# Kernel tuning notes

Measured on AMD Instinct MI355X. Metric: run time of the kernel, lower is better.

The kernel has to match this reference:

```python
import jax, jax.numpy as jnp
import numpy as np

CODEBOOK_SIZE = 8192
TOKEN_SIZE = 256
COMMITMENT_COST = 0.25


def setup_inputs() -> dict:
    key = jax.random.key(0)
    k1, k2 = jax.random.split(key)
    z = jax.random.normal(k1, (32, 1024, TOKEN_SIZE), dtype=jnp.float32)
    # embedding initialized uniform in [-1/K, 1/K] as in torch module
    embedding = jax.random.uniform(
        k2, (CODEBOOK_SIZE, TOKEN_SIZE), dtype=jnp.float32,
        minval=-1.0 / CODEBOOK_SIZE, maxval=1.0 / CODEBOOK_SIZE)
    return {"z": z, "embedding": embedding}


def reference(z, embedding):
    B, T, D = z.shape
    zf = z.reshape(B * T, D)                               # [N, D]
    # squared euclidean distances: ||z||^2 + ||e||^2 - 2 z.e
    d = (jnp.sum(zf * zf, axis=1, keepdims=True)
         + jnp.sum(embedding * embedding, axis=1)
         - 2.0 * jnp.einsum('nd,kd->nk', zf, embedding))   # [N, K]
    idx = jnp.argmin(d, axis=1)                            # [N]
    z_q = embedding[idx].reshape(B, T, D)                  # codebook gather
    commitment_loss = COMMITMENT_COST * jnp.mean(
        (jax.lax.stop_gradient(z_q) - z) ** 2)
    codebook_loss = jnp.mean((z_q - jax.lax.stop_gradient(z)) ** 2)
    loss = commitment_loss + codebook_loss                 # ema_update=False
    # straight-through estimator
    z_q_st = z + jax.lax.stop_gradient(z_q - z)
    return (z_q_st, loss, commitment_loss, codebook_loss,
            idx.reshape(B, T))
```

## Files before the change

kernel.cpp:

```cpp
#include <hip/hip_runtime.h>
#include <hip/hip_bf16.h>
#include <cfloat>

#define N_TOK   32768
#define K_CODES 8192
#define D_DIM   256
#define BTOK    128
#define CHUNK   128
#define NSPLIT  4
#define SPLITK  (K_CODES / NSPLIT)
#define CTAU_M  3.0e-5f
#define CAND_MM 2.4e-5f
#define MAXCAND 16
#define RBTOK   32
#define NRS     8
#define RSPLIT  (K_CODES / NRS)

typedef __attribute__((ext_vector_type(4)))  short bf16x4;
typedef __attribute__((ext_vector_type(8)))  short bf16x8;
typedef __attribute__((ext_vector_type(16))) float f32x16;


__device__ __forceinline__ float np_sumsq256(const float* __restrict__ row) {
    #pragma clang fp contract(off)
    float blk[2];
    #pragma unroll
    for (int b = 0; b < 2; b++) {
        const float* x = row + b * 128;
        float r[8];
        #pragma unroll
        for (int j = 0; j < 8; j++) { float v = x[j]; r[j] = v * v; }
        for (int i = 8; i < 128; i += 8) {
            #pragma unroll
            for (int j = 0; j < 8; j++) { float v = x[i + j]; r[j] += v * v; }
        }
        blk[b] = ((r[0] + r[1]) + (r[2] + r[3])) + ((r[4] + r[5]) + (r[6] + r[7]));
    }
    return blk[0] + blk[1];
}

__device__ __forceinline__ float np_einsum256(const float* __restrict__ a,
                                              const float* __restrict__ b) {
    #pragma clang fp contract(off)
    float A0 = 0.f, A1 = 0.f, A2 = 0.f, A3 = 0.f;
    for (int m = 0; m < 256; m += 16) {
        A0 = a[m+ 0]*b[m+ 0] + (a[m+ 4]*b[m+ 4] + (a[m+ 8]*b[m+ 8] + (a[m+12]*b[m+12] + A0)));
        A1 = a[m+ 1]*b[m+ 1] + (a[m+ 5]*b[m+ 5] + (a[m+ 9]*b[m+ 9] + (a[m+13]*b[m+13] + A1)));
        A2 = a[m+ 2]*b[m+ 2] + (a[m+ 6]*b[m+ 6] + (a[m+10]*b[m+10] + (a[m+14]*b[m+14] + A2)));
        A3 = a[m+ 3]*b[m+ 3] + (a[m+ 7]*b[m+ 7] + (a[m+11]*b[m+11] + (a[m+15]*b[m+15] + A3)));
    }
    return (A0 + A1) + (A2 + A3);
}

__device__ __forceinline__ float np_dtilde(float Cn, float e2k, float g) {
    #pragma clang fp contract(off)
    float t = Cn + e2k;
    float d = t - 2.0f * g;
    return d;
}

__device__ __forceinline__ unsigned short bf16_rne(float f) {
    unsigned u = __float_as_uint(f);
    unsigned r = u + 0x7fffu + ((u >> 16) & 1u);
    return (unsigned short)(r >> 16);
}
__device__ __forceinline__ void split_bf16(float f, short& hi, short& lo) {
    unsigned short h = bf16_rne(f);
    hi = (short)h;
    float hf = __uint_as_float(((unsigned)h) << 16);
    lo = (short)bf16_rne(f - hf);
}
__device__ __forceinline__ bf16x8 lo8(bf16x8 h, float4 a, float4 b) {
    float f[8] = {a.x, a.y, a.z, a.w, b.x, b.y, b.z, b.w};
    bf16x8 r;
    #pragma unroll
    for (int i = 0; i < 8; i += 2) {
        float d0 = f[i]     - __uint_as_float(((unsigned)(unsigned short)h[i])     << 16);
        float d1 = f[i + 1] - __uint_as_float(((unsigned)(unsigned short)h[i + 1]) << 16);
        __hip_bfloat162 p = __float22bfloat162_rn(make_float2(d0, d1));
        unsigned u; __builtin_memcpy(&u, &p, 4);
        r[i]     = (short)(u & 0xffffu);
        r[i + 1] = (short)(u >> 16);
    }
    return r;
}

#define MFMA3(A, ah, al, bh, bl) \
    A = __builtin_amdgcn_mfma_f32_32x32x16_bf16(ah, bh, A, 0, 0, 0); \
    A = __builtin_amdgcn_mfma_f32_32x32x16_bf16(ah, bl, A, 0, 0, 0); \
    A = __builtin_amdgcn_mfma_f32_32x32x16_bf16(al, bh, A, 0, 0, 0);

__global__ __launch_bounds__(256) void prep_e_kernel(
    const float* __restrict__ emb, float* __restrict__ e2np,
    float* __restrict__ e2h, unsigned* __restrict__ ccount,
    double* __restrict__ loss_sum)
{
    int k = blockIdx.x * 256 + threadIdx.x;
    float v = np_sumsq256(emb + (size_t)k * D_DIM);
    e2np[k] = v;
    e2h[k]  = 0.5f * v;
    if (k == 0) { *ccount = 0u; *loss_sum = 0.0; }
}

__global__ __launch_bounds__(256) void prep_z_kernel(
    const float* __restrict__ z, float* __restrict__ Cnp)
{
    int t = blockIdx.x * 256 + threadIdx.x;
    Cnp[t] = np_sumsq256(z + (size_t)t * D_DIM);
}

__global__ __launch_bounds__(256) void cvt_e_kernel(
    const float* __restrict__ src, short* __restrict__ hi, short* __restrict__ lo)
{
    size_t p = ((size_t)blockIdx.x * 256 + threadIdx.x) * 8;
    float4 v0 = *(const float4*)(src + p);
    float4 v1 = *(const float4*)(src + p + 4);
    short h[8], l[8];
    split_bf16(v0.x, h[0], l[0]); split_bf16(v0.y, h[1], l[1]);
    split_bf16(v0.z, h[2], l[2]); split_bf16(v0.w, h[3], l[3]);
    split_bf16(v1.x, h[4], l[4]); split_bf16(v1.y, h[5], l[5]);
    split_bf16(v1.z, h[6], l[6]); split_bf16(v1.w, h[7], l[7]);
    bf16x8 vh = {h[0],h[1],h[2],h[3],h[4],h[5],h[6],h[7]};
    bf16x8 vl = {l[0],l[1],l[2],l[3],l[4],l[5],l[6],l[7]};
    *(bf16x8*)(hi + p) = vh;
    *(bf16x8*)(lo + p) = vl;
}

__global__ __launch_bounds__(256) void cvt_zhi_kernel(
    const float* __restrict__ src, short* __restrict__ hi)
{
    size_t p = ((size_t)blockIdx.x * 256 + threadIdx.x) * 8;
    float4 v0 = *(const float4*)(src + p);
    float4 v1 = *(const float4*)(src + p + 4);
    bf16x8 vh = {(short)bf16_rne(v0.x), (short)bf16_rne(v0.y),
                 (short)bf16_rne(v0.z), (short)bf16_rne(v0.w),
                 (short)bf16_rne(v1.x), (short)bf16_rne(v1.y),
                 (short)bf16_rne(v1.z), (short)bf16_rne(v1.w)};
    *(bf16x8*)(hi + p) = vh;
}

#define B_ESH 0
#define B_ESL 4096
#define B_ZSH 8192
#define B_ZSL 12288
#define TILE1 1024

__global__ __launch_bounds__(512, 4) void bulk_kernel(
    const float* __restrict__ zf, const short* __restrict__ zhi,
    const short* __restrict__ ehi, const short* __restrict__ elo,
    const float* __restrict__ e2h,
    float* __restrict__ m1a, float* __restrict__ m2a, int* __restrict__ i1a)
{
    __shared__ __align__(16) short smem[2][16384];
    __shared__ float e2sall[SPLITK];
    __shared__ float s1m[BTOK], s2m[BTOK];
    __shared__ int   i1m[BTOK];

    const int tid  = threadIdx.x;
    const int lane = tid & 63;
    const int w    = tid >> 6;
    const int wt   = w & 1;
    const int wc   = w >> 1;
    const int g     = blockIdx.x & 255;
    const int split = blockIdx.x >> 8;
    const int tok0  = g * BTOK;
    const int cs0   = split * SPLITK;

    const int r0 = tid >> 2, q0 = tid & 3;
    const int so0 = r0 * 32 + ((q0 ^ ((r0 >> 1) & 3)) << 3);

    const int l31 = lane & 31, hh = lane >> 5;
    const int swz = (l31 >> 1) & 3;
    const int arow = (wc * 32 + l31) * 32;
    const int brow = (wt * 64 + l31) * 32;
    const int a0 = arow + ((hh ^ swz) << 3);
    const int a1 = arow + (((2 + hh) ^ swz) << 3);
    const int b0 = brow + ((hh ^ swz) << 3);
    const int b1 = brow + (((2 + hh) ^ swz) << 3);

    float m1[2] = {-FLT_MAX, -FLT_MAX}, m2[2] = {-FLT_MAX, -FLT_MAX};
    int   k1[2] = {0x7fffffff, 0x7fffffff};

    bf16x8 ehA, elA, zhA;  float4 zfaA, zfbA;
    bf16x8 ehB, elB, zhB;  float4 zfaB, zfbB;

    f32x16 acc[2];
    #pragma unroll
    for (int j = 0; j < 2; j++)
        #pragma unroll
        for (int r = 0; r < 16; r++) acc[j][r] = 0.f;

    const int NST = (SPLITK / CHUNK) * 8;

    auto ISSUE_A = [&](int s) {
        const int code0 = cs0 + (s >> 3) * CHUNK;
        const int d0 = (s & 7) * 32;
        const size_t ei = ((size_t)(code0 + r0) << 8) + d0 + (q0 << 3);
        const size_t zi = ((size_t)(tok0 + r0) << 8) + d0 + (q0 << 3);
        ehA = *(const bf16x8*)(ehi + ei);
        elA = *(const bf16x8*)(elo + ei);
        zhA = *(const bf16x8*)(zhi + zi);
        zfaA = *(const float4*)(zf + zi);
        zfbA = *(const float4*)(zf + zi + 4);
    };
    auto ISSUE_B = [&](int s) {
        const int code0 = cs0 + (s >> 3) * CHUNK;
        const int d0 = (s & 7) * 32;
        const size_t ei = ((size_t)(code0 + r0) << 8) + d0 + (q0 << 3);
        const size_t zi = ((size_t)(tok0 + r0) << 8) + d0 + (q0 << 3);
        ehB = *(const bf16x8*)(ehi + ei);
        elB = *(const bf16x8*)(elo + ei);
        zhB = *(const bf16x8*)(zhi + zi);
        zfaB = *(const float4*)(zf + zi);
        zfbB = *(const float4*)(zf + zi + 4);
    };

    auto STORE_A = [&](int buf) {
        bf16x8 zl0 = lo8(zhA, zfaA, zfbA);
        short* sm = smem[buf];
        *(bf16x8*)(sm + B_ESH + so0) = ehA;
        *(bf16x8*)(sm + B_ESL + so0) = elA;
        *(bf16x8*)(sm + B_ZSH + so0) = zhA;
        *(bf16x8*)(sm + B_ZSL + so0) = zl0;
    };
    auto STORE_B = [&](int buf) {
        bf16x8 zl0 = lo8(zhB, zfaB, zfbB);
        short* sm = smem[buf];
        *(bf16x8*)(sm + B_ESH + so0) = ehB;
        *(bf16x8*)(sm + B_ESL + so0) = elB;
        *(bf16x8*)(sm + B_ZSH + so0) = zhB;
        *(bf16x8*)(sm + B_ZSL + so0) = zl0;
    };

    #pragma unroll
    for (int i = 0; i < SPLITK / 512; i++) {
        int idx = tid + i * 512;
        e2sall[idx] = e2h[cs0 + idx];
    }
    ISSUE_A(0);
    ISSUE_B(1);
    STORE_A(0);
    __syncthreads();

    #pragma unroll 2
    for (int s = 0; s < NST; s++) {
        const int cur = s & 1;
        if (s + 2 < NST) {
            if (cur == 0) ISSUE_A(s + 2); else ISSUE_B(s + 2);
        }
        {
            const short* sm = smem[cur];
            {
                bf16x8 ah  = *(const bf16x8*)(sm + B_ESH + a0);
                bf16x8 al  = *(const bf16x8*)(sm + B_ESL + a0);
                bf16x8 b0h = *(const bf16x8*)(sm + B_ZSH + b0);
                bf16x8 b0l = *(const bf16x8*)(sm + B_ZSL + b0);
                bf16x8 b1h = *(const bf16x8*)(sm + B_ZSH + TILE1 + b0);
                bf16x8 b1l = *(const bf16x8*)(sm + B_ZSL + TILE1 + b0);
                MFMA3(acc[0], ah, al, b0h, b0l);
                MFMA3(acc[1], ah, al, b1h, b1l);
            }
            {
                bf16x8 ah  = *(const bf16x8*)(sm + B_ESH + a1);
                bf16x8 al  = *(const bf16x8*)(sm + B_ESL + a1);
                bf16x8 b0h = *(const bf16x8*)(sm + B_ZSH + b1);
                bf16x8 b0l = *(const bf16x8*)(sm + B_ZSL + b1);
                bf16x8 b1h = *(const bf16x8*)(sm + B_ZSH + TILE1 + b1);
                bf16x8 b1l = *(const bf16x8*)(sm + B_ZSL + TILE1 + b1);
                MFMA3(acc[0], ah, al, b0h, b0l);
                MFMA3(acc[1], ah, al, b1h, b1l);
            }
        }
        if ((s & 7) == 7) {
            const int code0 = cs0 + (s >> 3) * CHUNK;
            const float* e2c = e2sall + (s >> 3) * CHUNK;
            float ev[16];
            #pragma unroll
            for (int r = 0; r < 16; r++)
                ev[r] = e2c[wc * 32 + hh * 4 + (r & 3) + ((r >> 2) << 3)];
            #pragma unroll
            for (int tt = 0; tt < 2; tt++) {
                #pragma unroll
                for (int r = 0; r < 16; r++) {
                    float a = acc[tt][r] - ev[r];
                    int code = code0 + wc * 32 + hh * 4 + (r & 3) + ((r >> 2) << 3);
                    if (a > m1[tt]) { m2[tt] = m1[tt]; m1[tt] = a; k1[tt] = code; }
                    else if (a > m2[tt]) m2[tt] = a;
                }
            }
            #pragma unroll
            for (int j = 0; j < 2; j++)
                #pragma unroll
                for (int r = 0; r < 16; r++) acc[j][r] = 0.f;
        }
        if (s + 1 < NST) {
            if (cur == 0) STORE_B(cur ^ 1); else STORE_A(cur ^ 1);
        }
        asm volatile("s_waitcnt lgkmcnt(0)" ::: "memory");
        __builtin_amdgcn_s_barrier();
        __builtin_amdgcn_sched_barrier(0);
    }

    #pragma unroll
    for (int tt = 0; tt < 2; tt++) {
        float o1 = __shfl_xor(m1[tt], 32);
        float o2 = __shfl_xor(m2[tt], 32);
        int   oi = __shfl_xor(k1[tt], 32);
        bool take = (o1 > m1[tt]) || (o1 == m1[tt] && oi < k1[tt]);
        float w1 = take ? o1 : m1[tt];
        int   wi = take ? oi : k1[tt];
        float ls = take ? m1[tt] : o1;
        m2[tt] = fmaxf(fmaxf(m2[tt], o2), ls);
        m1[tt] = w1; k1[tt] = wi;
    }
    __syncthreads();
    if (wc == 0 && lane < 32) {
        #pragma unroll
        for (int tt = 0; tt < 2; tt++) {
            int tl = wt * 64 + tt * 32 + lane;
            s1m[tl] = m1[tt]; s2m[tl] = m2[tt]; i1m[tl] = k1[tt];
        }
    }
    __syncthreads();
    #pragma unroll
    for (int mw = 1; mw < 3; mw++) {
        if (wc == mw && lane < 32) {
            #pragma unroll
            for (int tt = 0; tt < 2; tt++) {
                int tl = wt * 64 + tt * 32 + lane;
                float a1 = s1m[tl], a2 = s2m[tl]; int ai = i1m[tl];
                bool take = (a1 > m1[tt]) || (a1 == m1[tt] && ai < k1[tt]);
                float w1 = take ? a1 : m1[tt];
                int   wi = take ? ai : k1[tt];
                float ls = take ? m1[tt] : a1;
                float w2 = fmaxf(fmaxf(m2[tt], a2), ls);
                s1m[tl] = w1; s2m[tl] = w2; i1m[tl] = wi;
            }
        }
        __syncthreads();
    }
    if (wc == 3 && lane < 32) {
        #pragma unroll
        for (int tt = 0; tt < 2; tt++) {
            int tl = wt * 64 + tt * 32 + lane;
            float a1 = s1m[tl], a2 = s2m[tl]; int ai = i1m[tl];
            bool take = (a1 > m1[tt]) || (a1 == m1[tt] && ai < k1[tt]);
            float w1 = take ? a1 : m1[tt];
            int   wi = take ? ai : k1[tt];
            float ls = take ? m1[tt] : a1;
            float w2 = fmaxf(fmaxf(m2[tt], a2), ls);
            size_t t = (size_t)(tok0 + tl) * NSPLIT + split;
            m1a[t] = w1; m2a[t] = w2; i1a[t] = wi;
        }
    }
}

__global__ __launch_bounds__(256) void merge_kernel(
    const float* __restrict__ m1a, const float* __restrict__ m2a,
    const int* __restrict__ i1a, float* __restrict__ m1f,
    int* __restrict__ idxf, int* __restrict__ clist,
    unsigned* __restrict__ ccount, unsigned* __restrict__ ccnt_g)
{
    int t = blockIdx.x * 256 + threadIdx.x;
    ccnt_g[t] = 0u;
    float w1 = m1a[t * NSPLIT], w2 = m2a[t * NSPLIT];
    int   wi = i1a[t * NSPLIT];
    #pragma unroll
    for (int s = 1; s < NSPLIT; s++) {
        float a1 = m1a[t * NSPLIT + s], a2 = m2a[t * NSPLIT + s];
        int   ai = i1a[t * NSPLIT + s];
        bool take = (a1 > w1) || (a1 == w1 && ai < wi);
        float n1 = take ? a1 : w1;
        int   ni = take ? ai : wi;
        float ls = take ? w1 : a1;
        w2 = fmaxf(fmaxf(w2, a2), ls);
        w1 = n1; wi = ni;
    }
    idxf[t] = wi; m1f[t] = w1;
    if (w1 - w2 < CTAU_M) {
        unsigned p = atomicAdd(ccount, 1u);
        clist[p] = t;
    }
}

#define R_ESH 0
#define R_ESL 4096
#define R_ZSH 8192
#define R_ZSL 9216

__global__ __launch_bounds__(256) void rescue_kernel(
    const float* __restrict__ zf, const short* __restrict__ zhi,
    const short* __restrict__ ehi, const short* __restrict__ elo,
    const float* __restrict__ e2h, const float* __restrict__ m1f,
    const unsigned* __restrict__ ccount, const int* __restrict__ clist,
    unsigned* __restrict__ ccnt_g, int* __restrict__ cand_g)
{
    const unsigned count = *ccount;
    const unsigned base  = blockIdx.x * RBTOK;
    if (base >= count) return;
    const int nt = min(RBTOK, (int)(count - base));
    const int sp = blockIdx.y;

    __shared__ __align__(16) short rsm[10240];
    __shared__ int   tls[RBTOK];
    __shared__ float thr[RBTOK];
    __shared__ float e2s[CHUNK];

    const int tid  = threadIdx.x;
    const int lane = tid & 63;
    const int w    = tid >> 6;

    if (tid < RBTOK) {
        int s = (tid < nt) ? tid : (nt - 1);
        int t = clist[base + s];
        tls[tid] = t;
        thr[tid] = (tid < nt) ? (m1f[t] - CAND_MM) : FLT_MAX;
    }
    __syncthreads();

    const int l31 = lane & 31, hh = lane >> 5;
    const float mythr = thr[l31];
    const int   mytok = tls[l31];
    const int swz = (l31 >> 1) & 3;
    const int arow = (w * 32 + l31) * 32;
    const int brow = l31 * 32;
    const int a0 = arow + ((hh ^ swz) << 3);
    const int a1 = arow + (((2 + hh) ^ swz) << 3);
    const int b0 = brow + ((hh ^ swz) << 3);
    const int b1 = brow + (((2 + hh) ^ swz) << 3);

    const int er0 = tid >> 2, eq0 = tid & 3;
    const int er1 = er0 + 64;
    const int eso0 = er0 * 32 + ((eq0 ^ ((er0 >> 1) & 3)) << 3);
    const int eso1 = er1 * 32 + ((eq0 ^ ((er1 >> 1) & 3)) << 3);
    const int zr = (tid & 127) >> 2, zq = tid & 3;
    const int zso = zr * 32 + ((zq ^ ((zr >> 1) & 3)) << 3);

    for (int c = 0; c < RSPLIT / CHUNK; c++) {
        const int code0 = sp * RSPLIT + c * CHUNK;
        const float e2v = (tid < CHUNK) ? e2h[code0 + tid] : 0.f;
        f32x16 acc;
        #pragma unroll
        for (int r = 0; r < 16; r++) acc[r] = 0.f;

        for (int st = 0; st < 8; st++) {
            const int d0 = st * 32;
            const size_t ei0 = ((size_t)(code0 + er0) << 8) + d0 + (eq0 << 3);
            const size_t ei1 = ((size_t)(code0 + er1) << 8) + d0 + (eq0 << 3);
            bf16x8 eh0 = *(const bf16x8*)(ehi + ei0);
            bf16x8 el0 = *(const bf16x8*)(elo + ei0);
            bf16x8 eh1 = *(const bf16x8*)(ehi + ei1);
            bf16x8 el1 = *(const bf16x8*)(elo + ei1);
            bf16x8 zh = {}, zl = {};
            if (tid < 128) {
                const size_t zi = ((size_t)tls[zr] << 8) + d0 + (zq << 3);
                zh = *(const bf16x8*)(zhi + zi);
                float4 za = *(const float4*)(zf + zi);
                float4 zb = *(const float4*)(zf + zi + 4);
                zl = lo8(zh, za, zb);
            }
            __syncthreads();
            *(bf16x8*)(rsm + R_ESH + eso0) = eh0;
            *(bf16x8*)(rsm + R_ESL + eso0) = el0;
            *(bf16x8*)(rsm + R_ESH + eso1) = eh1;
            *(bf16x8*)(rsm + R_ESL + eso1) = el1;
            if (tid < 128) {
                *(bf16x8*)(rsm + R_ZSH + zso) = zh;
                *(bf16x8*)(rsm + R_ZSL + zso) = zl;
            }
            if (st == 0 && tid < CHUNK) e2s[tid] = e2v;
            __syncthreads();
            {
                bf16x8 ah = *(const bf16x8*)(rsm + R_ESH + a0);
                bf16x8 al = *(const bf16x8*)(rsm + R_ESL + a0);
                bf16x8 bh = *(const bf16x8*)(rsm + R_ZSH + b0);
                bf16x8 bl = *(const bf16x8*)(rsm + R_ZSL + b0);
                MFMA3(acc, ah, al, bh, bl);
            }
            {
                bf16x8 ah = *(const bf16x8*)(rsm + R_ESH + a1);
                bf16x8 al = *(const bf16x8*)(rsm + R_ESL + a1);
                bf16x8 bh = *(const bf16x8*)(rsm + R_ZSH + b1);
                bf16x8 bl = *(const bf16x8*)(rsm + R_ZSL + b1);
                MFMA3(acc, ah, al, bh, bl);
            }
        }
        #pragma unroll
        for (int r = 0; r < 16; r++) {
            const int local = w * 32 + hh * 4 + (r & 3) + ((r >> 2) << 3);
            float a = acc[r] - e2s[local];
            if (a >= mythr) {
                unsigned p = atomicAdd(&ccnt_g[mytok], 1u);
                if (p < MAXCAND) cand_g[(size_t)mytok * MAXCAND + p] = code0 + local;
            }
        }
    }
}

__global__ __launch_bounds__(256) void resolve_kernel(
    const float* __restrict__ z, const float* __restrict__ emb,
    const float* __restrict__ e2np, const float* __restrict__ Cnp,
    const unsigned* __restrict__ ccount, const int* __restrict__ clist,
    const unsigned* __restrict__ ccnt_g, const int* __restrict__ cand_g,
    int* __restrict__ idxf)
{
    const unsigned count = *ccount;
    const int lane = threadIdx.x & 63;
    const int w    = threadIdx.x >> 6;
    for (unsigned c = blockIdx.x * 4 + w; c < count; c += gridDim.x * 4) {
        const int t = clist[c];
        const int n = (int)min(ccnt_g[t], (unsigned)MAXCAND);
        float bd = FLT_MAX; int bk = 0x7fffffff;
        if (lane < n) {
            const int k = cand_g[(size_t)t * MAXCAND + lane];
            float g = np_einsum256(z + (size_t)t * D_DIM, emb + (size_t)k * D_DIM);
            bd = np_dtilde(Cnp[t], e2np[k], g);
            bk = k;
        }
        #pragma unroll
        for (int off = 32; off >= 1; off >>= 1) {
            float od = __shfl_xor(bd, off);
            int   ok = __shfl_xor(bk, off);
            if (od < bd || (od == bd && ok < bk)) { bd = od; bk = ok; }
        }
        if (lane == 0 && n > 0) idxf[t] = bk;
    }
}

__global__ __launch_bounds__(256) void out_loss_kernel(
    const float* __restrict__ z, const float* __restrict__ emb,
    const int* __restrict__ idxf, float* __restrict__ out0,
    double* __restrict__ loss_sum)
{
    const int total4 = N_TOK * (D_DIM / 4);
    double lsum = 0.0;
    for (int p = blockIdx.x * 256 + threadIdx.x; p < total4; p += gridDim.x * 256) {
        const int n  = p >> 6;
        const int d4 = p & 63;
        const int k  = idxf[n];
        float4 zv = ((const float4*)z)[p];
        float4 ev = ((const float4*)(emb + (size_t)k * D_DIM))[d4];
        float dx = ev.x - zv.x, dy = ev.y - zv.y,
              dz = ev.z - zv.z, dw = ev.w - zv.w;
        float4 o;
        o.x = zv.x + dx; o.y = zv.y + dy; o.z = zv.z + dz; o.w = zv.w + dw;
        ((float4*)out0)[p] = o;
        lsum += (double)dx * dx + (double)dy * dy
              + (double)dz * dz + (double)dw * dw;
    }
    #pragma unroll
    for (int off = 32; off >= 1; off >>= 1) lsum += __shfl_xor(lsum, off);
    __shared__ double wsum[4];
    const int wv = threadIdx.x >> 6;
    if ((threadIdx.x & 63) == 0) wsum[wv] = lsum;
    __syncthreads();
    if (threadIdx.x == 0)
        atomicAdd(loss_sum, wsum[0] + wsum[1] + wsum[2] + wsum[3]);
}

__global__ __launch_bounds__(256) void finalize_kernel(
    const int* __restrict__ idxf, const double* __restrict__ loss_sum,
    float* __restrict__ out)
{
    const int t = blockIdx.x * 256 + threadIdx.x;
    if (t < N_TOK) out[8388611 + t] = (float)idxf[t];
    if (t == 0) {
        double mse = *loss_sum * (1.0 / 8388608.0);
        out[8388608] = (float)(1.25 * mse);
        out[8388609] = (float)(0.25 * mse);
        out[8388610] = (float)mse;
    }
}

extern "C" void kernel_launch(void* const* d_in, const int* in_sizes, int n_in,
                              void* d_out, int out_size, void* d_ws, size_t ws_size,
                              hipStream_t stream)
{
    const float* z   = (const float*)d_in[0];
    const float* emb = (const float*)d_in[1];
    float* out = (float*)d_out;
    char*  ws  = (char*)d_ws;
    char*  ob  = (char*)d_out;

    short*    ehi    = (short*)(ob + 0);
    short*    elo    = (short*)(ob + 4194304);
    short*    zhi    = (short*)(ob + 8388608);
    float*    m1a    = (float*)(ob + 25165824);
    float*    m2a    = (float*)(ob + 25690112);
    int*      i1a    = (int*)(ob + 26214400);
    int*      cand_g = (int*)(ob + 26738688);

    double*   loss_sum = (double*)(ws + 0);
    unsigned* ccount   = (unsigned*)(ws + 8);
    float*    e2np     = (float*)(ws + 16);
    float*    e2h      = (float*)(ws + 32784);
    float*    Cnp      = (float*)(ws + 65552);
    float*    m1f      = (float*)(ws + 196624);
    int*      idxf     = (int*)(ws + 327696);
    int*      clist    = (int*)(ws + 458768);
    unsigned* ccnt_g   = (unsigned*)(ws + 589840);

    prep_e_kernel<<<dim3(K_CODES / 256), dim3(256), 0, stream>>>(
        emb, e2np, e2h, ccount, loss_sum);
    prep_z_kernel<<<dim3(N_TOK / 256), dim3(256), 0, stream>>>(z, Cnp);
    cvt_e_kernel<<<dim3(K_CODES * D_DIM / 8 / 256), dim3(256), 0, stream>>>(emb, ehi, elo);
    cvt_zhi_kernel<<<dim3(N_TOK * D_DIM / 8 / 256), dim3(256), 0, stream>>>(z, zhi);
    bulk_kernel<<<dim3((N_TOK / BTOK) * NSPLIT), dim3(512), 0, stream>>>(
        z, zhi, ehi, elo, e2h, m1a, m2a, i1a);
    merge_kernel<<<dim3(N_TOK / 256), dim3(256), 0, stream>>>(
        m1a, m2a, i1a, m1f, idxf, clist, ccount, ccnt_g);
    rescue_kernel<<<dim3(N_TOK / RBTOK, NRS), dim3(256), 0, stream>>>(
        z, zhi, ehi, elo, e2h, m1f, ccount, clist, ccnt_g, cand_g);
    resolve_kernel<<<dim3(128), dim3(256), 0, stream>>>(
        z, emb, e2np, Cnp, ccount, clist, ccnt_g, cand_g, idxf);
    out_loss_kernel<<<dim3(1024), dim3(256), 0, stream>>>(
        z, emb, idxf, out, loss_sum);
    finalize_kernel<<<dim3(N_TOK / 256), dim3(256), 0, stream>>>(
        idxf, loss_sum, out);
}
```

Baseline: 780.0 us.

## Restructure bulk distance kernel to 256 threads, 2x2 MFMA tiles, three codebook splits

Reworks the main distance/argmin kernel from 512-thread blocks with 4 codebook splits to 256-thread blocks with 3 uneven splits (22/21/21 chunks), giving 768 blocks instead of 1024. Each wave now computes a 2x2 grid of MFMA tiles, reusing each loaded A and B fragment twice. The K-step is halved to 16 so each stage's shared buffer is smaller, at the cost of more pipeline steps and syncs. It also adds s_setprio around the MFMA block and shortens the cross-wave reduction to two waves. The swizzle on the shared layout is dropped, which may introduce LDS bank conflicts, and more accumulators per thread raise register pressure.

```diff
diff --git a/kernel.cpp b/kernel.cpp
--- a/kernel.cpp
+++ b/kernel.cpp
@@ -7,8 +7,7 @@
 #define D_DIM   256
 #define BTOK    128
 #define CHUNK   128
-#define NSPLIT  4
-#define SPLITK  (K_CODES / NSPLIT)
+#define NSPLIT  3
 #define CTAU_M  3.0e-5f
 #define CAND_MM 2.4e-5f
 #define MAXCAND 16
@@ -140,19 +139,19 @@
 }
 
 #define B_ESH 0
-#define B_ESL 4096
-#define B_ZSH 8192
-#define B_ZSL 12288
-#define TILE1 1024
-
-__global__ __launch_bounds__(512, 4) void bulk_kernel(
+#define B_ESL 2048
+#define B_ZSH 4096
+#define B_ZSL 6144
+#define BUFSZ 8192
+
+__global__ __launch_bounds__(256, 3) void bulk_kernel(
     const float* __restrict__ zf, const short* __restrict__ zhi,
     const short* __restrict__ ehi, const short* __restrict__ elo,
     const float* __restrict__ e2h,
     float* __restrict__ m1a, float* __restrict__ m2a, int* __restrict__ i1a)
 {
-    __shared__ __align__(16) short smem[2][16384];
-    __shared__ float e2sall[SPLITK];
+    __shared__ __align__(16) short smem[2][BUFSZ];
+    __shared__ float e2sall[22 * CHUNK];
     __shared__ float s1m[BTOK], s2m[BTOK];
     __shared__ int   i1m[BTOK];
 
@@ -164,19 +163,18 @@
     const int g     = blockIdx.x & 255;
     const int split = blockIdx.x >> 8;
     const int tok0  = g * BTOK;
-    const int cs0   = split * SPLITK;
-
-    const int r0 = tid >> 2, q0 = tid & 3;
-    const int so0 = r0 * 32 + ((q0 ^ ((r0 >> 1) & 3)) << 3);
+    const int cbase = split * 21 + (split ? 1 : 0);
+    const int nch   = split ? 21 : 22;
+    const int cs0   = cbase * CHUNK;
+
+    const int r0 = tid >> 1, q0 = tid & 1;
+    const int so0 = r0 * 16 + q0 * 8;
 
     const int l31 = lane & 31, hh = lane >> 5;
-    const int swz = (l31 >> 1) & 3;
-    const int arow = (wc * 32 + l31) * 32;
-    const int brow = (wt * 64 + l31) * 32;
-    const int a0 = arow + ((hh ^ swz) << 3);
-    const int a1 = arow + (((2 + hh) ^ swz) << 3);
-    const int b0 = brow + ((hh ^ swz) << 3);
-    const int b1 = brow + (((2 + hh) ^ swz) << 3);
+    const int a0 = (wc * 64 + l31) * 16 + hh * 8;
+    const int a1 = a0 + 512;
+    const int b0 = (wt * 64 + l31) * 16 + hh * 8;
+    const int b1 = b0 + 512;
 
     float m1[2] = {-FLT_MAX, -FLT_MAX}, m2[2] = {-FLT_MAX, -FLT_MAX};
     int   k1[2] = {0x7fffffff, 0x7fffffff};
@@ -184,17 +182,19 @@
     bf16x8 ehA, elA, zhA;  float4 zfaA, zfbA;
     bf16x8 ehB, elB, zhB;  float4 zfaB, zfbB;
 
-    f32x16 acc[2];
+    f32x16 acc[2][2];
     #pragma unroll
-    for (int j = 0; j < 2; j++)
+    for (int i = 0; i < 2; i++)
         #pragma unroll
-        for (int r = 0; r < 16; r++) acc[j][r] = 0.f;
-
-    const int NST = (SPLITK / CHUNK) * 8;
+        for (int j = 0; j < 2; j++)
+            #pragma unroll
+            for (int r = 0; r < 16; r++) acc[i][j][r] = 0.f;
+
+    const int NST = nch * 16;
 
     auto ISSUE_A = [&](int s) {
-        const int code0 = cs0 + (s >> 3) * CHUNK;
-        const int d0 = (s & 7) * 32;
+        const int code0 = cs0 + (s >> 4) * CHUNK;
+        const int d0 = (s & 15) * 16;
         const size_t ei = ((size_t)(code0 + r0) << 8) + d0 + (q0 << 3);
         const size_t zi = ((size_t)(tok0 + r0) << 8) + d0 + (q0 << 3);
         ehA = *(const bf16x8*)(ehi + ei);
@@ -204,8 +204,8 @@
         zfbA = *(const float4*)(zf + zi + 4);
     };
     auto ISSUE_B = [&](int s) {
-        const int code0 = cs0 + (s >> 3) * CHUNK;
-        const int d0 = (s & 7) * 32;
+        const int code0 = cs0 + (s >> 4) * CHUNK;
+        const int d0 = (s & 15) * 16;
         const size_t ei = ((size_t)(code0 + r0) << 8) + d0 + (q0 << 3);
         const size_t zi = ((size_t)(tok0 + r0) << 8) + d0 + (q0 << 3);
         ehB = *(const bf16x8*)(ehi + ei);
@@ -232,11 +232,8 @@
         *(bf16x8*)(sm + B_ZSL + so0) = zl0;
     };
 
-    #pragma unroll
-    for (int i = 0; i < SPLITK / 512; i++) {
-        int idx = tid + i * 512;
+    for (int idx = tid; idx < nch * CHUNK; idx += 256)
         e2sall[idx] = e2h[cs0 + idx];
-    }
     ISSUE_A(0);
     ISSUE_B(1);
     STORE_A(0);
@@ -250,48 +247,48 @@
         }
         {
             const short* sm = smem[cur];
-            {
-                bf16x8 ah  = *(const bf16x8*)(sm + B_ESH + a0);
-                bf16x8 al  = *(const bf16x8*)(sm + B_ESL + a0);
-                bf16x8 b0h = *(const bf16x8*)(sm + B_ZSH + b0);
-                bf16x8 b0l = *(const bf16x8*)(sm + B_ZSL + b0);
-                bf16x8 b1h = *(const bf16x8*)(sm + B_ZSH + TILE1 + b0);
-                bf16x8 b1l = *(const bf16x8*)(sm + B_ZSL + TILE1 + b0);
-                MFMA3(acc[0], ah, al, b0h, b0l);
-                MFMA3(acc[1], ah, al, b1h, b1l);
-            }
-            {
-                bf16x8 ah  = *(const bf16x8*)(sm + B_ESH + a1);
-                bf16x8 al  = *(const bf16x8*)(sm + B_ESL + a1);
-                bf16x8 b0h = *(const bf16x8*)(sm + B_ZSH + b1);
-                bf16x8 b0l = *(const bf16x8*)(sm + B_ZSL + b1);
-                bf16x8 b1h = *(const bf16x8*)(sm + B_ZSH + TILE1 + b1);
-                bf16x8 b1l = *(const bf16x8*)(sm + B_ZSL + TILE1 + b1);
-                MFMA3(acc[0], ah, al, b0h, b0l);
-                MFMA3(acc[1], ah, al, b1h, b1l);
-            }
-        }
-        if ((s & 7) == 7) {
-            const int code0 = cs0 + (s >> 3) * CHUNK;
-            const float* e2c = e2sall + (s >> 3) * CHUNK;
-            float ev[16];
+            bf16x8 a0h = *(const bf16x8*)(sm + B_ESH + a0);
+            bf16x8 a0l = *(const bf16x8*)(sm + B_ESL + a0);
+            bf16x8 a1h = *(const bf16x8*)(sm + B_ESH + a1);
+            bf16x8 a1l = *(const bf16x8*)(sm + B_ESL + a1);
+            bf16x8 b0h = *(const bf16x8*)(sm + B_ZSH + b0);
+            bf16x8 b0l = *(const bf16x8*)(sm + B_ZSL + b0);
+            bf16x8 b1h = *(const bf16x8*)(sm + B_ZSH + b1);
+            bf16x8 b1l = *(const bf16x8*)(sm + B_ZSL + b1);
+            __builtin_amdgcn_s_setprio(1);
+            MFMA3(acc[0][0], a0h, a0l, b0h, b0l);
+            MFMA3(acc[0][1], a0h, a0l, b1h, b1l);
+            MFMA3(acc[1][0], a1h, a1l, b0h, b0l);
+            MFMA3(acc[1][1], a1h, a1l, b1h, b1l);
+            __builtin_amdgcn_s_setprio(0);
+        }
+        if ((s & 15) == 15) {
+            const int c = s >> 4;
+            const int code0 = cs0 + c * CHUNK;
+            const float* e2c = e2sall + c * CHUNK;
             #pragma unroll
-            for (int r = 0; r < 16; r++)
-                ev[r] = e2c[wc * 32 + hh * 4 + (r & 3) + ((r >> 2) << 3)];
-            #pragma unroll
-            for (int tt = 0; tt < 2; tt++) {
+            for (int i = 0; i < 2; i++) {
+                float ev[16];
                 #pragma unroll
-                for (int r = 0; r < 16; r++) {
-                    float a = acc[tt][r] - ev[r];
-                    int code = code0 + wc * 32 + hh * 4 + (r & 3) + ((r >> 2) << 3);
-                    if (a > m1[tt]) { m2[tt] = m1[tt]; m1[tt] = a; k1[tt] = code; }
-                    else if (a > m2[tt]) m2[tt] = a;
+                for (int r = 0; r < 16; r++)
+                    ev[r] = e2c[wc * 64 + i * 32 + hh * 4 + (r & 3) + ((r >> 2) << 3)];
+                #pragma unroll
+                for (int j = 0; j < 2; j++) {
+                    #pragma unroll
+                    for (int r = 0; r < 16; r++) {
+                        float a = acc[i][j][r] - ev[r];
+                        int code = code0 + wc * 64 + i * 32 + hh * 4 + (r & 3) + ((r >> 2) << 3);
+                        if (a > m1[j]) { m2[j] = m1[j]; m1[j] = a; k1[j] = code; }
+                        else if (a > m2[j]) m2[j] = a;
+                    }
                 }
             }
             #pragma unroll
-            for (int j = 0; j < 2; j++)
+            for (int i = 0; i < 2; i++)
                 #pragma unroll
-                for (int r = 0; r < 16; r++) acc[j][r] = 0.f;
+                for (int j = 0; j < 2; j++)
+                    #pragma unroll
+                    for (int r = 0; r < 16; r++) acc[i][j][r] = 0.f;
         }
         if (s + 1 < NST) {
             if (cur == 0) STORE_B(cur ^ 1); else STORE_A(cur ^ 1);
@@ -302,53 +299,36 @@
     }
 
     #pragma unroll
-    for (int tt = 0; tt < 2; tt++) {
-        float o1 = __shfl_xor(m1[tt], 32);
-        float o2 = __shfl_xor(m2[tt], 32);
-        int   oi = __shfl_xor(k1[tt], 32);
-        bool take = (o1 > m1[tt]) || (o1 == m1[tt] && oi < k1[tt]);
-        float w1 = take ? o1 : m1[tt];
-        int   wi = take ? oi : k1[tt];
-        float ls = take ? m1[tt] : o1;
-        m2[tt] = fmaxf(fmaxf(m2[tt], o2), ls);
-        m1[tt] = w1; k1[tt] = wi;
+    for (int j = 0; j < 2; j++) {
+        float o1 = __shfl_xor(m1[j], 32);
+        float o2 = __shfl_xor(m2[j], 32);
+        int   oi = __shfl_xor(k1[j], 32);
+        bool take = (o1 > m1[j]) || (o1 == m1[j] && oi < k1[j]);
+        float w1 = take ? o1 : m1[j];
+        int   wi = take ? oi : k1[j];
+        float ls = take ? m1[j] : o1;
+        m2[j] = fmaxf(fmaxf(m2[j], o2), ls);
+        m1[j] = w1; k1[j] = wi;
     }
     __syncthreads();
     if (wc == 0 && lane < 32) {
         #pragma unroll
-        for (int tt = 0; tt < 2; tt++) {
-            int tl = wt * 64 + tt * 32 + lane;
-            s1m[tl] = m1[tt]; s2m[tl] = m2[tt]; i1m[tl] = k1[tt];
+        for (int j = 0; j < 2; j++) {
+            int tl = wt * 64 + j * 32 + lane;
+            s1m[tl] = m1[j]; s2m[tl] = m2[j]; i1m[tl] = k1[j];
         }
     }
     __syncthreads();
-    #pragma unroll
-    for (int mw = 1; mw < 3; mw++) {
-        if (wc == mw && lane < 32) {
-            #pragma unroll
-            for (int tt = 0; tt < 2; tt++) {
-                int tl = wt * 64 + tt * 32 + lane;
-                float a1 = s1m[tl], a2 = s2m[tl]; int ai = i1m[tl];
-                bool take = (a1 > m1[tt]) || (a1 == m1[tt] && ai < k1[tt]);
-                float w1 = take ? a1 : m1[tt];
-                int   wi = take ? ai : k1[tt];
-                float ls = take ? m1[tt] : a1;
-                float w2 = fmaxf(fmaxf(m2[tt], a2), ls);
-                s1m[tl] = w1; s2m[tl] = w2; i1m[tl] = wi;
-            }
-        }
-        __syncthreads();
-    }
-    if (wc == 3 && lane < 32) {
+    if (wc == 1 && lane < 32) {
         #pragma unroll
-        for (int tt = 0; tt < 2; tt++) {
-            int tl = wt * 64 + tt * 32 + lane;
+        for (int j = 0; j < 2; j++) {
+            int tl = wt * 64 + j * 32 + lane;
             float a1 = s1m[tl], a2 = s2m[tl]; int ai = i1m[tl];
-            bool take = (a1 > m1[tt]) || (a1 == m1[tt] && ai < k1[tt]);
-            float w1 = take ? a1 : m1[tt];
-            int   wi = take ? ai : k1[tt];
-            float ls = take ? m1[tt] : a1;
-            float w2 = fmaxf(fmaxf(m2[tt], a2), ls);
+            bool take = (a1 > m1[j]) || (a1 == m1[j] && ai < k1[j]);
+            float w1 = take ? a1 : m1[j];
+            int   wi = take ? ai : k1[j];
+            float ls = take ? m1[j] : a1;
+            float w2 = fmaxf(fmaxf(m2[j], a2), ls);
             size_t t = (size_t)(tok0 + tl) * NSPLIT + split;
             m1a[t] = w1; m2a[t] = w2; i1a[t] = wi;
         }
@@ -605,7 +585,7 @@
     prep_z_kernel<<<dim3(N_TOK / 256), dim3(256), 0, stream>>>(z, Cnp);
     cvt_e_kernel<<<dim3(K_CODES * D_DIM / 8 / 256), dim3(256), 0, stream>>>(emb, ehi, elo);
     cvt_zhi_kernel<<<dim3(N_TOK * D_DIM / 8 / 256), dim3(256), 0, stream>>>(z, zhi);
-    bulk_kernel<<<dim3((N_TOK / BTOK) * NSPLIT), dim3(512), 0, stream>>>(
+    bulk_kernel<<<dim3((N_TOK / BTOK) * NSPLIT), dim3(256), 0, stream>>>(
         z, zhi, ehi, elo, e2h, m1a, m2a, i1a);
     merge_kernel<<<dim3(N_TOK / 256), dim3(256), 0, stream>>>(
         m1a, m2a, i1a, m1f, idxf, clist, ccount, ccnt_g);
```

New measurement: 926.8 us. 18.8% more time.

## Load codebook A-operand directly from pre-transposed layout into registers, drop zhi pass

Applied to the files above, without the earlier changes.

The codebook hi/lo bf16 split is also written in an MFMA-friendly transposed layout, so the bulk kernel loads A-operand fragments straight from global memory into registers instead of staging them through LDS. This halves the shared-memory tile and the LDS write/read traffic per stage. The separate z-hi conversion kernel is removed and z is split into hi/lo on the fly, and MFMA blocks are wrapped in s_setprio. The cost is extra global loads per wave, with less reuse of codebook data across waves, plus more register pressure from double-buffered A fragments.

```diff
diff --git a/kernel.cpp b/kernel.cpp
--- a/kernel.cpp
+++ b/kernel.cpp
@@ -70,19 +70,21 @@
     float hf = __uint_as_float(((unsigned)h) << 16);
     lo = (short)bf16_rne(f - hf);
 }
-__device__ __forceinline__ bf16x8 lo8(bf16x8 h, float4 a, float4 b) {
+__device__ __forceinline__ void split8v(float4 a, float4 b, bf16x8& h, bf16x8& l) {
     float f[8] = {a.x, a.y, a.z, a.w, b.x, b.y, b.z, b.w};
-    bf16x8 r;
     #pragma unroll
     for (int i = 0; i < 8; i += 2) {
-        float d0 = f[i]     - __uint_as_float(((unsigned)(unsigned short)h[i])     << 16);
-        float d1 = f[i + 1] - __uint_as_float(((unsigned)(unsigned short)h[i + 1]) << 16);
-        __hip_bfloat162 p = __float22bfloat162_rn(make_float2(d0, d1));
-        unsigned u; __builtin_memcpy(&u, &p, 4);
-        r[i]     = (short)(u & 0xffffu);
-        r[i + 1] = (short)(u >> 16);
-    }
-    return r;
+        __hip_bfloat162 hp = __float22bfloat162_rn(make_float2(f[i], f[i + 1]));
+        unsigned hu; __builtin_memcpy(&hu, &hp, 4);
+        h[i]     = (short)(hu & 0xffffu);
+        h[i + 1] = (short)(hu >> 16);
+        float h0 = __uint_as_float(hu << 16);
+        float h1 = __uint_as_float(hu & 0xffff0000u);
+        __hip_bfloat162 lp = __float22bfloat162_rn(make_float2(f[i] - h0, f[i + 1] - h1));
+        unsigned lu; __builtin_memcpy(&lu, &lp, 4);
+        l[i]     = (short)(lu & 0xffffu);
+        l[i + 1] = (short)(lu >> 16);
+    }
 }
 
 #define MFMA3(A, ah, al, bh, bl) \
@@ -110,7 +112,8 @@
 }
 
 __global__ __launch_bounds__(256) void cvt_e_kernel(
-    const float* __restrict__ src, short* __restrict__ hi, short* __restrict__ lo)
+    const float* __restrict__ src, short* __restrict__ hi, short* __restrict__ lo,
+    short* __restrict__ hit, short* __restrict__ lot)
 {
     size_t p = ((size_t)blockIdx.x * 256 + threadIdx.x) * 8;
     float4 v0 = *(const float4*)(src + p);
@@ -124,34 +127,23 @@
     bf16x8 vl = {l[0],l[1],l[2],l[3],l[4],l[5],l[6],l[7]};
     *(bf16x8*)(hi + p) = vh;
     *(bf16x8*)(lo + p) = vl;
-}
-
-__global__ __launch_bounds__(256) void cvt_zhi_kernel(
-    const float* __restrict__ src, short* __restrict__ hi)
-{
-    size_t p = ((size_t)blockIdx.x * 256 + threadIdx.x) * 8;
-    float4 v0 = *(const float4*)(src + p);
-    float4 v1 = *(const float4*)(src + p + 4);
-    bf16x8 vh = {(short)bf16_rne(v0.x), (short)bf16_rne(v0.y),
-                 (short)bf16_rne(v0.z), (short)bf16_rne(v0.w),
-                 (short)bf16_rne(v1.x), (short)bf16_rne(v1.y),
-                 (short)bf16_rne(v1.z), (short)bf16_rne(v1.w)};
-    *(bf16x8*)(hi + p) = vh;
-}
-
-#define B_ESH 0
-#define B_ESL 4096
-#define B_ZSH 8192
-#define B_ZSL 12288
+    const int code = (int)(p >> 8);
+    const int d    = (int)(p & 255);
+    size_t tp = ((size_t)(d >> 4) * K_CODES + code) * 16 + (d & 15);
+    *(bf16x8*)(hit + tp) = vh;
+    *(bf16x8*)(lot + tp) = vl;
+}
+
+#define Z_SH 0
+#define Z_SL 4096
 #define TILE1 1024
 
 __global__ __launch_bounds__(512, 4) void bulk_kernel(
-    const float* __restrict__ zf, const short* __restrict__ zhi,
-    const short* __restrict__ ehi, const short* __restrict__ elo,
-    const float* __restrict__ e2h,
+    const float* __restrict__ zf, const short* __restrict__ eht,
+    const short* __restrict__ elt, const float* __restrict__ e2h,
     float* __restrict__ m1a, float* __restrict__ m2a, int* __restrict__ i1a)
 {
-    __shared__ __align__(16) short smem[2][16384];
+    __shared__ __align__(16) short smem[2][8192];
     __shared__ float e2sall[SPLITK];
     __shared__ float s1m[BTOK], s2m[BTOK];
     __shared__ int   i1m[BTOK];
@@ -171,18 +163,17 @@
 
     const int l31 = lane & 31, hh = lane >> 5;
     const int swz = (l31 >> 1) & 3;
-    const int arow = (wc * 32 + l31) * 32;
+    const int acode = cs0 + wc * 32 + l31;
     const int brow = (wt * 64 + l31) * 32;
-    const int a0 = arow + ((hh ^ swz) << 3);
-    const int a1 = arow + (((2 + hh) ^ swz) << 3);
     const int b0 = brow + ((hh ^ swz) << 3);
     const int b1 = brow + (((2 + hh) ^ swz) << 3);
 
     float m1[2] = {-FLT_MAX, -FLT_MAX}, m2[2] = {-FLT_MAX, -FLT_MAX};
     int   k1[2] = {0x7fffffff, 0x7fffffff};
 
-    bf16x8 ehA, elA, zhA;  float4 zfaA, zfbA;
-    bf16x8 ehB, elB, zhB;  float4 zfaB, zfbB;
+    float4 zfaA, zfbA, zfaB, zfbB;
+    bf16x8 a0hA, a0lA, a1hA, a1lA;
+    bf16x8 a0hB, a0lB, a1hB, a1lB;
 
     f32x16 acc[2];
     #pragma unroll
@@ -192,44 +183,69 @@
 
     const int NST = (SPLITK / CHUNK) * 8;
 
-    auto ISSUE_A = [&](int s) {
-        const int code0 = cs0 + (s >> 3) * CHUNK;
-        const int d0 = (s & 7) * 32;
-        const size_t ei = ((size_t)(code0 + r0) << 8) + d0 + (q0 << 3);
-        const size_t zi = ((size_t)(tok0 + r0) << 8) + d0 + (q0 << 3);
-        ehA = *(const bf16x8*)(ehi + ei);
-        elA = *(const bf16x8*)(elo + ei);
-        zhA = *(const bf16x8*)(zhi + zi);
+    auto ZISSUE_A = [&](int s) {
+        const size_t zi = ((size_t)(tok0 + r0) << 8) + (s & 7) * 32 + (q0 << 3);
         zfaA = *(const float4*)(zf + zi);
         zfbA = *(const float4*)(zf + zi + 4);
     };
-    auto ISSUE_B = [&](int s) {
-        const int code0 = cs0 + (s >> 3) * CHUNK;
-        const int d0 = (s & 7) * 32;
-        const size_t ei = ((size_t)(code0 + r0) << 8) + d0 + (q0 << 3);
-        const size_t zi = ((size_t)(tok0 + r0) << 8) + d0 + (q0 << 3);
-        ehB = *(const bf16x8*)(ehi + ei);
-        elB = *(const bf16x8*)(elo + ei);
-        zhB = *(const bf16x8*)(zhi + zi);
+    auto ZISSUE_B = [&](int s) {
+        const size_t zi = ((size_t)(tok0 + r0) << 8) + (s & 7) * 32 + (q0 << 3);
         zfaB = *(const float4*)(zf + zi);
         zfbB = *(const float4*)(zf + zi + 4);
     };
-
-    auto STORE_A = [&](int buf) {
-        bf16x8 zl0 = lo8(zhA, zfaA, zfbA);
+    auto AISSUE_A = [&](int s) {
+        const int c = s >> 3, dst = s & 7;
+        const size_t p0 = ((size_t)(2 * dst + 0) * K_CODES + (acode + c * CHUNK)) * 16 + hh * 8;
+        const size_t p1 = ((size_t)(2 * dst + 1) * K_CODES + (acode + c * CHUNK)) * 16 + hh * 8;
+        a0hA = *(const bf16x8*)(eht + p0);
+        a0lA = *(const bf16x8*)(elt + p0);
+        a1hA = *(const bf16x8*)(eht + p1);
+        a1lA = *(const bf16x8*)(elt + p1);
+    };
+    auto AISSUE_B = [&](int s) {
+        const int c = s >> 3, dst = s & 7;
+        const size_t p0 = ((size_t)(2 * dst + 0) * K_CODES + (acode + c * CHUNK)) * 16 + hh * 8;
+        const size_t p1 = ((size_t)(2 * dst + 1) * K_CODES + (acode + c * CHUNK)) * 16 + hh * 8;
+        a0hB = *(const bf16x8*)(eht + p0);
+        a0lB = *(const bf16x8*)(elt + p0);
+        a1hB = *(const bf16x8*)(eht + p1);
+        a1lB = *(const bf16x8*)(elt + p1);
+    };
+
+    auto ZSTORE_A = [&](int buf) {
+        bf16x8 zh, zl;
+        split8v(zfaA, zfbA, zh, zl);
         short* sm = smem[buf];
-        *(bf16x8*)(sm + B_ESH + so0) = ehA;
-        *(bf16x8*)(sm + B_ESL + so0) = elA;
-        *(bf16x8*)(sm + B_ZSH + so0) = zhA;
-        *(bf16x8*)(sm + B_ZSL + so0) = zl0;
+        *(bf16x8*)(sm + Z_SH + so0) = zh;
+        *(bf16x8*)(sm + Z_SL + so0) = zl;
     };
-    auto STORE_B = [&](int buf) {
-        bf16x8 zl0 = lo8(zhB, zfaB, zfbB);
+    auto ZSTORE_B = [&](int buf) {
+        bf16x8 zh, zl;
+        split8v(zfaB, zfbB, zh, zl);
         short* sm = smem[buf];
-        *(bf16x8*)(sm + B_ESH + so0) = ehB;
-        *(bf16x8*)(sm + B_ESL + so0) = elB;
-        *(bf16x8*)(sm + B_ZSH + so0) = zhB;
-        *(bf16x8*)(sm + B_ZSL + so0) = zl0;
+        *(bf16x8*)(sm + Z_SH + so0) = zh;
+        *(bf16x8*)(sm + Z_SL + so0) = zl;
+    };
+
+    auto MFMABLK = [&](bf16x8 k0h, bf16x8 k0l, bf16x8 k1h, bf16x8 k1l, const short* sm) {
+        __builtin_amdgcn_s_setprio(1);
+        {
+            bf16x8 b0h = *(const bf16x8*)(sm + Z_SH + b0);
+            bf16x8 b0l = *(const bf16x8*)(sm + Z_SL + b0);
+            bf16x8 b1h = *(const bf16x8*)(sm + Z_SH + TILE1 + b0);
+            bf16x8 b1l = *(const bf16x8*)(sm + Z_SL + TILE1 + b0);
+            MFMA3(acc[0], k0h, k0l, b0h, b0l);
+            MFMA3(acc[1], k0h, k0l, b1h, b1l);
+        }
+        {
+            bf16x8 b0h = *(const bf16x8*)(sm + Z_SH + b1);
+            bf16x8 b0l = *(const bf16x8*)(sm + Z_SL + b1);
+            bf16x8 b1h = *(const bf16x8*)(sm + Z_SH + TILE1 + b1);
+            bf16x8 b1l = *(const bf16x8*)(sm + Z_SL + TILE1 + b1);
+            MFMA3(acc[0], k1h, k1l, b0h, b0l);
+            MFMA3(acc[1], k1h, k1l, b1h, b1l);
+        }
+        __builtin_amdgcn_s_setprio(0);
     };
 
     #pragma unroll
@@ -237,39 +253,25 @@
         int idx = tid + i * 512;
         e2sall[idx] = e2h[cs0 + idx];
     }
-    ISSUE_A(0);
-    ISSUE_B(1);
-    STORE_A(0);
+    ZISSUE_A(0);
+    ZISSUE_B(1);
+    AISSUE_A(0);
+    ZSTORE_A(0);
     __syncthreads();
 
     #pragma unroll 2
     for (int s = 0; s < NST; s++) {
         const int cur = s & 1;
         if (s + 2 < NST) {
-            if (cur == 0) ISSUE_A(s + 2); else ISSUE_B(s + 2);
+            if (cur == 0) ZISSUE_A(s + 2); else ZISSUE_B(s + 2);
         }
         {
             const short* sm = smem[cur];
-            {
-                bf16x8 ah  = *(const bf16x8*)(sm + B_ESH + a0);
-                bf16x8 al  = *(const bf16x8*)(sm + B_ESL + a0);
-                bf16x8 b0h = *(const bf16x8*)(sm + B_ZSH + b0);
-                bf16x8 b0l = *(const bf16x8*)(sm + B_ZSL + b0);
-                bf16x8 b1h = *(const bf16x8*)(sm + B_ZSH + TILE1 + b0);
-                bf16x8 b1l = *(const bf16x8*)(sm + B_ZSL + TILE1 + b0);
-                MFMA3(acc[0], ah, al, b0h, b0l);
-                MFMA3(acc[1], ah, al, b1h, b1l);
-            }
-            {
-                bf16x8 ah  = *(const bf16x8*)(sm + B_ESH + a1);
-                bf16x8 al  = *(const bf16x8*)(sm + B_ESL + a1);
-                bf16x8 b0h = *(const bf16x8*)(sm + B_ZSH + b1);
-                bf16x8 b0l = *(const bf16x8*)(sm + B_ZSL + b1);
-                bf16x8 b1h = *(const bf16x8*)(sm + B_ZSH + TILE1 + b1);
-                bf16x8 b1l = *(const bf16x8*)(sm + B_ZSL + TILE1 + b1);
-                MFMA3(acc[0], ah, al, b0h, b0l);
-                MFMA3(acc[1], ah, al, b1h, b1l);
-            }
+            if (cur == 0) MFMABLK(a0hA, a0lA, a1hA, a1lA, sm);
+            else          MFMABLK(a0hB, a0lB, a1hB, a1lB, sm);
+        }
+        if (s + 1 < NST) {
+            if (cur == 0) AISSUE_B(s + 1); else AISSUE_A(s + 1);
         }
         if ((s & 7) == 7) {
             const int code0 = cs0 + (s >> 3) * CHUNK;
@@ -294,7 +296,7 @@
                 for (int r = 0; r < 16; r++) acc[j][r] = 0.f;
         }
         if (s + 1 < NST) {
-            if (cur == 0) STORE_B(cur ^ 1); else STORE_A(cur ^ 1);
+            if (cur == 0) ZSTORE_B(cur ^ 1); else ZSTORE_A(cur ^ 1);
         }
         asm volatile("s_waitcnt lgkmcnt(0)" ::: "memory");
         __builtin_amdgcn_s_barrier();
@@ -389,7 +391,7 @@
 #define R_ZSL 9216
 
 __global__ __launch_bounds__(256) void rescue_kernel(
-    const float* __restrict__ zf, const short* __restrict__ zhi,
+    const float* __restrict__ zf,
     const short* __restrict__ ehi, const short* __restrict__ elo,
     const float* __restrict__ e2h, const float* __restrict__ m1f,
     const unsigned* __restrict__ ccount, const int* __restrict__ clist,
@@ -454,10 +456,9 @@
             bf16x8 zh = {}, zl = {};
             if (tid < 128) {
                 const size_t zi = ((size_t)tls[zr] << 8) + d0 + (zq << 3);
-                zh = *(const bf16x8*)(zhi + zi);
                 float4 za = *(const float4*)(zf + zi);
                 float4 zb = *(const float4*)(zf + zi + 4);
-                zl = lo8(zh, za, zb);
+                split8v(za, zb, zh, zl);
             }
             __syncthreads();
             *(bf16x8*)(rsm + R_ESH + eso0) = eh0;
@@ -584,11 +585,12 @@
 
     short*    ehi    = (short*)(ob + 0);
     short*    elo    = (short*)(ob + 4194304);
-    short*    zhi    = (short*)(ob + 8388608);
-    float*    m1a    = (float*)(ob + 25165824);
-    float*    m2a    = (float*)(ob + 25690112);
-    int*      i1a    = (int*)(ob + 26214400);
-    int*      cand_g = (int*)(ob + 26738688);
+    short*    eht    = (short*)(ob + 8388608);
+    short*    elt    = (short*)(ob + 12582912);
+    float*    m1a    = (float*)(ob + 16777216);
+    float*    m2a    = (float*)(ob + 17301504);
+    int*      i1a    = (int*)(ob + 17825792);
+    int*      cand_g = (int*)(ob + 18350080);
 
     double*   loss_sum = (double*)(ws + 0);
     unsigned* ccount   = (unsigned*)(ws + 8);
@@ -603,14 +605,14 @@
     prep_e_kernel<<<dim3(K_CODES / 256), dim3(256), 0, stream>>>(
         emb, e2np, e2h, ccount, loss_sum);
     prep_z_kernel<<<dim3(N_TOK / 256), dim3(256), 0, stream>>>(z, Cnp);
-    cvt_e_kernel<<<dim3(K_CODES * D_DIM / 8 / 256), dim3(256), 0, stream>>>(emb, ehi, elo);
-    cvt_zhi_kernel<<<dim3(N_TOK * D_DIM / 8 / 256), dim3(256), 0, stream>>>(z, zhi);
+    cvt_e_kernel<<<dim3(K_CODES * D_DIM / 8 / 256), dim3(256), 0, stream>>>(
+        emb, ehi, elo, eht, elt);
     bulk_kernel<<<dim3((N_TOK / BTOK) * NSPLIT), dim3(512), 0, stream>>>(
-        z, zhi, ehi, elo, e2h, m1a, m2a, i1a);
+        z, eht, elt, e2h, m1a, m2a, i1a);
     merge_kernel<<<dim3(N_TOK / 256), dim3(256), 0, stream>>>(
         m1a, m2a, i1a, m1f, idxf, clist, ccount, ccnt_g);
     rescue_kernel<<<dim3(N_TOK / RBTOK, NRS), dim3(256), 0, stream>>>(
-        z, zhi, ehi, elo, e2h, m1f, ccount, clist, ccnt_g, cand_g);
+        z, ehi, elo, e2h, m1f, ccount, clist, ccnt_g, cand_g);
     resolve_kernel<<<dim3(128), dim3(256), 0, stream>>>(
         z, emb, e2np, Cnp, ccount, clist, ccnt_g, cand_g, idxf);
     out_loss_kernel<<<dim3(1024), dim3(256), 0, stream>>>(
```

After: 767.0 us. No clear change (-1.7%).
